# Performance work log

Hardware: AMD Instinct MI355X
Metric: run time of the kernel (lower is better)

The kernel has to match this reference:

```python
import jax, jax.numpy as jnp
import numpy as np
import math

N_HEAD = 16
HEAD_DIM = 64
LN_EPS = 1e-5
TEMP = 1.0

def _layernorm(x, scale, bias):
    # normalize over last dim (head_dim)
    mu = jnp.mean(x, axis=-1, keepdims=True)
    var = jnp.mean(jnp.square(x - mu), axis=-1, keepdims=True)
    return (x - mu) / jnp.sqrt(var + LN_EPS) * scale + bias

def setup_inputs() -> dict:
    key = jax.random.key(0)
    ks = jax.random.split(key, 3)
    B, S, C = 4, 2048, 1024
    x = jax.random.normal(ks[0], (B, S, C), dtype=jnp.float32)
    w_qkv = jax.random.normal(ks[1], (C, 3 * C), dtype=jnp.float32) * (C ** -0.5)
    w_proj = jax.random.normal(ks[2], (C, C), dtype=jnp.float32) * (C ** -0.5)
    return {
        "x": x,
        "w_qkv": w_qkv,
        "w_proj": w_proj,
        "q_scale": jnp.ones((HEAD_DIM,), jnp.float32),
        "q_bias": jnp.zeros((HEAD_DIM,), jnp.float32),
        "k_scale": jnp.ones((HEAD_DIM,), jnp.float32),
        "k_bias": jnp.zeros((HEAD_DIM,), jnp.float32),
    }

def reference(x, w_qkv, w_proj, q_scale, q_bias, k_scale, k_bias):
    B, S, C = x.shape
    H, D = N_HEAD, HEAD_DIM
    # qkv projection -> [B,S,3,H,D] -> [3,B,H,S,D]
    qkv = (x @ w_qkv).reshape(B, S, 3, H, D).transpose(2, 0, 3, 1, 4)
    q = _layernorm(qkv[0], q_scale, q_bias)
    k = _layernorm(qkv[1], k_scale, k_bias)
    v = qkv[2]
    # temperature-scaled logits, stable softmax
    inv = 1.0 / (math.sqrt(D) * max(TEMP, 1e-6))
    logits = jnp.einsum('bhqd,bhkd->bhqk', q, k) * inv
    att = jax.nn.softmax(logits, axis=-1)
    # entropy stats (track_stats=True path)
    s_raw = -jnp.sum(att * jnp.log(att + 1e-9), axis=-1)  # [B,H,S]
    batch_entropies = jnp.mean(s_raw / math.log(S), axis=(1, 2))  # [B]
    out = jnp.einsum('bhqk,bhkd->bhqd', att, v).transpose(0, 2, 1, 3).reshape(B, S, C)
    return out @ w_proj, batch_entropies
```

## Files before the change

kernel.cpp:

```cpp
#include <hip/hip_runtime.h>
#include <hip/hip_bf16.h>
#include <math.h>

#define CB 4
#define CS 2048
#define CC 1024
#define CH 16
#define CD 64
#define CBS (CB*CS)

typedef unsigned short u16;
typedef __bf16 bf16x8 __attribute__((ext_vector_type(8)));
typedef float f32x4 __attribute__((ext_vector_type(4)));
typedef float f32x16 __attribute__((ext_vector_type(16)));
typedef unsigned short u16x4 __attribute__((ext_vector_type(4)));
typedef unsigned short u16x8 __attribute__((ext_vector_type(8)));

__device__ __forceinline__ u16 f2bf(float f){
  union { float f; unsigned u; } v; v.f = f;
  unsigned r = v.u + 0x7FFFu + ((v.u >> 16) & 1u);
  return (u16)(r >> 16);
}
__device__ __forceinline__ unsigned pack2bf(float a, float b){
  __hip_bfloat162 h = __float22bfloat162_rn(make_float2(a, b));
  union { __hip_bfloat162 h; unsigned u; } c; c.h = h; return c.u;
}
__device__ __forceinline__ f32x4 mfma16(bf16x8 a, bf16x8 b, f32x4 c){
  return __builtin_amdgcn_mfma_f32_16x16x32_bf16(a, b, c, 0, 0, 0);
}
__device__ __forceinline__ f32x16 mfma32(bf16x8 a, bf16x8 b, f32x16 c){
  return __builtin_amdgcn_mfma_f32_32x32x16_bf16(a, b, c, 0, 0, 0);
}
__device__ __forceinline__ void gload16(const u16* g, u16* lds_base_uniform){
  __builtin_amdgcn_global_load_lds(
      (const __attribute__((address_space(1))) unsigned int*)g,
      (__attribute__((address_space(3))) unsigned int*)lds_base_uniform, 16, 0, 0);
}

__global__ __launch_bounds__(256) void convert_x_kernel(
    const float* __restrict__ x, u16* __restrict__ xb, float* __restrict__ zero4){
  if (blockIdx.x == 0 && threadIdx.x < 4) zero4[threadIdx.x] = 0.0f;
  size_t i = ((size_t)blockIdx.x*256 + threadIdx.x)*8;
  float4 a = *(const float4*)(x+i);
  float4 b = *(const float4*)(x+i+4);
  u16x8 o = { f2bf(a.x),f2bf(a.y),f2bf(a.z),f2bf(a.w),
              f2bf(b.x),f2bf(b.y),f2bf(b.z),f2bf(b.w) };
  *(u16x8*)(xb+i) = o;
}

template<int K, int N>
__global__ __launch_bounds__(256) void transpose_convert_kernel(
    const float* __restrict__ w, u16* __restrict__ wt){
  __shared__ u16 tile[64][65];
  const int nb = N/64;
  int tk0 = (blockIdx.x / nb) * 64;
  int tn0 = (blockIdx.x % nb) * 64;
  int t = threadIdx.x;
  for (int i = 0; i < 4; i++) {
    int r = i*16 + (t>>4);
    int c = (t&15)*4;
    float4 v = *(const float4*)(w + (size_t)(tk0+r)*N + tn0 + c);
    tile[c+0][r]=f2bf(v.x); tile[c+1][r]=f2bf(v.y);
    tile[c+2][r]=f2bf(v.z); tile[c+3][r]=f2bf(v.w);
  }
  __syncthreads();
  for (int i = 0; i < 4; i++) {
    int r = i*16 + (t>>4);
    int c = (t&15)*4;
    u16x4 o = { tile[r][c+0], tile[r][c+1], tile[r][c+2], tile[r][c+3] };
    *(u16x4*)(wt + (size_t)(tn0+r)*K + tk0 + c) = o;
  }
}

__global__ __launch_bounds__(256) void transpose_v_kernel(
    const u16* __restrict__ vb, u16* __restrict__ vtb){
  __shared__ u16 tile[64][72];
  int bh = blockIdx.x >> 5;
  int st = blockIdx.x & 31;
  int t = threadIdx.x;
  const u16* src = vb + (size_t)bh*CS*CD + (size_t)st*64*CD;
  int r = t>>2, c = (t&3)*16;
  *(u16x8*)&tile[r][c]   = *(const u16x8*)(src + (size_t)r*CD + c);
  *(u16x8*)&tile[r][c+8] = *(const u16x8*)(src + (size_t)r*CD + c + 8);
  __syncthreads();
  int d = t>>2, s = (t&3)*16;
  u16x8 o0, o1;
  for (int j=0;j<8;j++){ o0[j] = tile[s+j][d]; o1[j] = tile[s+8+j][d]; }
  u16* dst = vtb + (size_t)bh*CD*CS + (size_t)d*CS + st*64 + s;
  *(u16x8*)dst = o0;
  *(u16x8*)(dst+8) = o1;
}

__global__ __launch_bounds__(256, 2) void gemm_qkv_ln_kernel(
    const u16* __restrict__ xb, const u16* __restrict__ wqkvT,
    const float* __restrict__ qsc, const float* __restrict__ qbi,
    const float* __restrict__ ksc, const float* __restrict__ kbi,
    u16* __restrict__ qb, u16* __restrict__ kb, u16* __restrict__ vb){
  __shared__ u16 al[128*64];
  __shared__ u16 bl[128*64];
  int t = threadIdx.x;
  int wv = t >> 6, lane = t & 63, lo = lane & 15, q4 = lane >> 4;
  int m0 = blockIdx.x * 128;
  int n0 = blockIdx.y * 128;
  int srow = lane >> 3, scol = (lane & 7) * 8;
  const u16* ag = xb    + (size_t)(m0 + srow)*CC + scol;
  const u16* bg = wqkvT + (size_t)(n0 + srow)*CC + scol;

  f32x4 acc[2][8];
  for (int i=0;i<2;i++) for (int j=0;j<8;j++) acc[i][j] = (f32x4){0.f,0.f,0.f,0.f};

  for (int kk = 0; kk < 16; kk++){
    int k0 = kk * 64;
    for (int i = 0; i < 4; i++){
      int inst = i*4 + wv;
      gload16(ag + (size_t)inst*8*CC + k0, al + inst*512);
      gload16(bg + (size_t)inst*8*CC + k0, bl + inst*512);
    }
    __syncthreads();
    for (int ksI = 0; ksI < 2; ksI++){
      int koff = ksI*32 + q4*8;
      bf16x8 a0 = *(const bf16x8*)&al[(wv*32      + lo)*64 + koff];
      bf16x8 a1 = *(const bf16x8*)&al[(wv*32 + 16 + lo)*64 + koff];
      for (int nt=0; nt<8; nt++){
        bf16x8 b = *(const bf16x8*)&bl[(nt*16 + lo)*64 + koff];
        acc[0][nt] = mfma16(a0, b, acc[0][nt]);
        acc[1][nt] = mfma16(a1, b, acc[1][nt]);
      }
    }
    __syncthreads();
  }

  int three = n0 >> 10;
  int h0 = (n0 & 1023) >> 6;
  const float* scp = (three == 0) ? qsc : ksc;
  const float* bip = (three == 0) ? qbi : kbi;
  float outscale = (three == 0) ? 0.125f : 1.0f;
  u16* dst = (three == 0) ? qb : (three == 1 ? kb : vb);

  for (int rt = 0; rt < 2; rt++){
    int tg = m0 + wv*32 + rt*16 + q4*4;
    for (int hf = 0; hf < 2; hf++){
      int h = h0 + hf;
      for (int r = 0; r < 4; r++){
        int token = tg + r;
        int bb = token >> 11, ss = token & (CS-1);
        size_t base = (((size_t)(bb*CH + h))*CS + ss)*CD;
        if (three < 2){
          float s1 = 0.f, s2 = 0.f;
          for (int j=0;j<4;j++){ float v = acc[rt][hf*4+j][r]; s1 += v; s2 += v*v; }
          for (int off=8; off>=1; off>>=1){
            s1 += __shfl_xor(s1, off, 16);
            s2 += __shfl_xor(s2, off, 16);
          }
          float mean = s1 * (1.f/64.f);
          float var  = s2 * (1.f/64.f) - mean*mean;
          float rstd = rsqrtf(var + 1e-5f);
          for (int j=0;j<4;j++){
            int d = j*16 + lo;
            float v = (acc[rt][hf*4+j][r] - mean) * rstd * scp[d] + bip[d];
            dst[base + d] = f2bf(v * outscale);
          }
        } else {
          for (int j=0;j<4;j++){
            int d = j*16 + lo;
            dst[base + d] = f2bf(acc[rt][hf*4+j][r]);
          }
        }
      }
    }
  }
}

__global__ __launch_bounds__(256, 3) void attention_kernel(
    const u16* __restrict__ qb, const u16* __restrict__ kb,
    const u16* __restrict__ vtb, u16* __restrict__ attnb, float* __restrict__ ent){
  __shared__ __align__(16) u16 kl[2][64*64];
  __shared__ __align__(16) u16 vl[2][64*64];
  __shared__ __align__(16) u16 pl[4][32][72];
  __shared__ __align__(16) float zl[4][32];
  int t = threadIdx.x;
  int wv = t >> 6, lane = t & 63;
  int col = lane & 31, hi = lane >> 5;
  int n = blockIdx.x;
  int xc = n & 7, j = n >> 3;
  int bh = xc + 8*(j >> 4);
  int qt = j & 15;
  int bI = bh >> 4;
  int q0w = qt*128 + wv*32;
  const u16* qbp = qb  + (size_t)bh * CS * CD;
  const u16* kbp = kb  + (size_t)bh * CS * CD;
  const u16* vbp = vtb + (size_t)bh * CD * CS;

  int srow  = lane >> 3;
  int sslot = (lane & 7) ^ srow;

  bf16x8 qf[4];
  for (int ks=0;ks<4;ks++)
    qf[ks] = *(const bf16x8*)(qbp + (size_t)(q0w + col)*CD + ks*16 + hi*8);

  f32x16 o[2];
  for (int nt=0;nt<2;nt++) for (int i=0;i<16;i++) o[nt][i] = 0.f;
  float zacc = 0.f, tacc = 0.f;

  for (int c=0;c<2;c++){
    int chunk = wv*2 + c;
    int row = chunk*8 + srow;
    gload16(kbp + (size_t)row*CD + sslot*8, &kl[0][chunk*512]);
    gload16(vbp + (size_t)row*CS + sslot*8, &vl[0][chunk*512]);
  }

  const int cshift = (col & 7);

  for (int it = 0; it < 32; it++){
    const int cur = it & 1, nxt = cur ^ 1;
    __syncthreads();
    if (it < 31){
      int skn = (it+1)*64;
      for (int c=0;c<2;c++){
        int chunk = wv*2 + c;
        int row = chunk*8 + srow;
        gload16(kbp + (size_t)(skn + row)*CD + sslot*8, &kl[nxt][chunk*512]);
        gload16(vbp + (size_t)row*CS + skn + sslot*8, &vl[nxt][chunk*512]);
      }
    }

    bf16x8 kfr[2][4], vfr[2][4];
    for (int mt=0;mt<2;mt++)
      for (int ks=0;ks<4;ks++)
        kfr[mt][ks] = *(const bf16x8*)&kl[cur][(mt*32+col)*64 + (((2*ks+hi)^cshift)<<3)];
    for (int nt=0;nt<2;nt++)
      for (int ks=0;ks<4;ks++)
        vfr[nt][ks] = *(const bf16x8*)&vl[cur][(nt*32+col)*64 + (((2*ks+hi)^cshift)<<3)];

    f32x16 sf[2];
    for (int mt=0;mt<2;mt++) for (int i=0;i<16;i++) sf[mt][i] = 0.f;
    for (int ks=0;ks<4;ks++){
      sf[0] = mfma32(kfr[0][ks], qf[ks], sf[0]);
      sf[1] = mfma32(kfr[1][ks], qf[ks], sf[1]);
    }

    for (int mt=0;mt<2;mt++){
      for (int g=0; g<4; g++){
        float l0 = sf[mt][g*4+0], l1 = sf[mt][g*4+1],
              l2 = sf[mt][g*4+2], l3 = sf[mt][g*4+3];
        float p0=__expf(l0), p1=__expf(l1), p2=__expf(l2), p3=__expf(l3);
        zacc += (p0+p1)+(p2+p3);
        tacc += (p0*l0+p1*l1)+(p2*l2+p3*l3);
        union { u16x4 v; unsigned u[2]; } pk;
        pk.u[0] = pack2bf(p0, p1);
        pk.u[1] = pack2bf(p2, p3);
        *(u16x4*)&pl[wv][col][mt*32 + g*8 + hi*4] = pk.v;
      }
    }

    for (int ks=0;ks<4;ks++){
      bf16x8 ap = *(const bf16x8*)&pl[wv][col][ks*16 + hi*8];
      o[0] = mfma32(ap, vfr[0][ks], o[0]);
      o[1] = mfma32(ap, vfr[1][ks], o[1]);
    }
  }

  float z2 = zacc + __shfl_xor(zacc, 32);
  float t2 = tacc + __shfl_xor(tacc, 32);
  float invz = 1.f / z2;
  if (hi == 0) zl[wv][col] = invz;

  float srowv = __logf(z2) - t2 * invz;
  float ev = (hi == 0) ? srowv : 0.f;
  for (int off=1; off<=32; off<<=1) ev += __shfl_xor(ev, off);
  if (lane == 0){
    float entscale = 1.0f / ((float)CH * (float)CS * logf((float)CS));
    atomicAdd(&ent[bI], ev * entscale);
  }

  u16* obase = attnb + ((size_t)bh*CS + q0w)*CD;
  for (int nt=0;nt<2;nt++){
    for (int g=0;g<4;g++){
      f32x4 iz = *(const f32x4*)&zl[wv][g*8 + hi*4];
      for (int r=0;r<4;r++){
        int qrow = 8*g + 4*hi + r;
        obase[(size_t)qrow*CD + nt*32 + col] = f2bf(o[nt][g*4+r] * iz[r]);
      }
    }
  }
}

__global__ __launch_bounds__(256, 2) void gemm_out_kernel(
    const u16* __restrict__ attnH, const u16* __restrict__ wprojT,
    float* __restrict__ out){
  __shared__ u16 al[128*64];
  __shared__ u16 bl[128*64];
  int t = threadIdx.x;
  int wv = t >> 6, lane = t & 63, lo = lane & 15, q4 = lane >> 4;
  int m0 = blockIdx.x * 128;
  int n0 = blockIdx.y * 128;
  int b  = m0 >> 11, s0 = m0 & (CS-1);
  int srow = lane >> 3, scol = (lane & 7) * 8;
  const u16* bg = wprojT + (size_t)(n0 + srow)*CC + scol;

  f32x4 acc[2][8];
  for (int i=0;i<2;i++) for (int j=0;j<8;j++) acc[i][j] = (f32x4){0.f,0.f,0.f,0.f};

  for (int kk = 0; kk < 16; kk++){
    const u16* abase = attnH + ((size_t)(b*CH + kk)*CS + s0 + srow)*CD + scol;
    for (int i = 0; i < 4; i++){
      int inst = i*4 + wv;
      gload16(abase + (size_t)inst*8*CD, al + inst*512);
      gload16(bg + (size_t)inst*8*CC + kk*64, bl + inst*512);
    }
    __syncthreads();
    for (int ksI = 0; ksI < 2; ksI++){
      int koff = ksI*32 + q4*8;
      bf16x8 a0 = *(const bf16x8*)&al[(wv*32      + lo)*64 + koff];
      bf16x8 a1 = *(const bf16x8*)&al[(wv*32 + 16 + lo)*64 + koff];
      for (int nt=0; nt<8; nt++){
        bf16x8 b2 = *(const bf16x8*)&bl[(nt*16 + lo)*64 + koff];
        acc[0][nt] = mfma16(a0, b2, acc[0][nt]);
        acc[1][nt] = mfma16(a1, b2, acc[1][nt]);
      }
    }
    __syncthreads();
  }

  for (int rt=0;rt<2;rt++){
    for (int r=0;r<4;r++){
      int row = m0 + wv*32 + rt*16 + q4*4 + r;
      for (int nt=0;nt<8;nt++)
        out[(size_t)row*CC + n0 + nt*16 + lo] = acc[rt][nt][r];
    }
  }
}

extern "C" void kernel_launch(void* const* d_in, const int* in_sizes, int n_in,
                              void* d_out, int out_size, void* d_ws, size_t ws_size,
                              hipStream_t stream) {
  const float* x      = (const float*)d_in[0];
  const float* w_qkv  = (const float*)d_in[1];
  const float* w_proj = (const float*)d_in[2];
  const float* q_scale= (const float*)d_in[3];
  const float* q_bias = (const float*)d_in[4];
  const float* k_scale= (const float*)d_in[5];
  const float* k_bias = (const float*)d_in[6];
  float* out = (float*)d_out;
  float* ent = out + (size_t)CBS * CC;

  u16* xb     = (u16*)d_ws;
  u16* wqkvT  = xb     + (size_t)CBS*CC;
  u16* wprojT = wqkvT  + (size_t)3*CC*CC;
  u16* qb     = wprojT + (size_t)CC*CC;
  u16* kb     = qb + (size_t)CB*CH*CS*CD;
  u16* vb     = kb + (size_t)CB*CH*CS*CD;
  u16* vbT    = xb;
  u16* attn   = vb;

  convert_x_kernel<<<dim3(CBS*CC/(256*8)), 256, 0, stream>>>(x, xb, ent);
  transpose_convert_kernel<CC, 3*CC><<<dim3((CC/64)*(3*CC/64)), 256, 0, stream>>>(w_qkv, wqkvT);
  transpose_convert_kernel<CC, CC><<<dim3((CC/64)*(CC/64)), 256, 0, stream>>>(w_proj, wprojT);
  gemm_qkv_ln_kernel<<<dim3(CBS/128, 3*CC/128), 256, 0, stream>>>(
      xb, wqkvT, q_scale, q_bias, k_scale, k_bias, qb, kb, vb);
  transpose_v_kernel<<<dim3(CB*CH*(CS/64)), 256, 0, stream>>>(vb, vbT);
  attention_kernel<<<dim3(CB*CH*(CS/128)), 256, 0, stream>>>(qb, kb, vbT, attn, ent);
  gemm_out_kernel<<<dim3(CBS/128, CC/128), 256, 0, stream>>>(attn, wprojT, out);
}
```

Measured before the change: 355.4 us.

## Keep P in registers via permlane32 swap, use exp2 with folded log2e

Removes the per-wave LDS staging buffer for attention probabilities. The bf16 P fragments are now rearranged between lane halves with permlane32_swap so they feed the PV MFMA directly from registers. The log2(e) factor is folded into the q scaling so the kernel can call hardware exp2 and log2, with the entropy rescaled by ln2. Freeing LDS lets launch bounds rise from 3 to 4 blocks per SM, at some risk of register pressure.

```diff
diff --git a/kernel.cpp b/kernel.cpp
--- a/kernel.cpp
+++ b/kernel.cpp
@@ -15,6 +15,7 @@
 typedef float f32x16 __attribute__((ext_vector_type(16)));
 typedef unsigned short u16x4 __attribute__((ext_vector_type(4)));
 typedef unsigned short u16x8 __attribute__((ext_vector_type(8)));
+typedef unsigned u32x2 __attribute__((ext_vector_type(2)));
 
 __device__ __forceinline__ u16 f2bf(float f){
   union { float f; unsigned u; } v; v.f = f;
@@ -134,7 +135,7 @@
   int h0 = (n0 & 1023) >> 6;
   const float* scp = (three == 0) ? qsc : ksc;
   const float* bip = (three == 0) ? qbi : kbi;
-  float outscale = (three == 0) ? 0.125f : 1.0f;
+  float outscale = (three == 0) ? 0.125f * 1.44269504088896f : 1.0f;
   u16* dst = (three == 0) ? qb : (three == 1 ? kb : vb);
 
   for (int rt = 0; rt < 2; rt++){
@@ -171,12 +172,11 @@
   }
 }
 
-__global__ __launch_bounds__(256, 3) void attention_kernel(
+__global__ __launch_bounds__(256, 4) void attention_kernel(
     const u16* __restrict__ qb, const u16* __restrict__ kb,
     const u16* __restrict__ vtb, u16* __restrict__ attnb, float* __restrict__ ent){
   __shared__ __align__(16) u16 kl[2][64*64];
   __shared__ __align__(16) u16 vl[2][64*64];
-  __shared__ __align__(16) u16 pl[4][32][72];
   __shared__ __align__(16) float zl[4][32];
   int t = threadIdx.x;
   int wv = t >> 6, lane = t & 63;
@@ -240,23 +240,32 @@
     }
 
     for (int mt=0;mt<2;mt++){
-      for (int g=0; g<4; g++){
-        float l0 = sf[mt][g*4+0], l1 = sf[mt][g*4+1],
-              l2 = sf[mt][g*4+2], l3 = sf[mt][g*4+3];
-        float p0=__expf(l0), p1=__expf(l1), p2=__expf(l2), p3=__expf(l3);
-        zacc += (p0+p1)+(p2+p3);
-        tacc += (p0*l0+p1*l1)+(p2*l2+p3*l3);
-        union { u16x4 v; unsigned u[2]; } pk;
-        pk.u[0] = pack2bf(p0, p1);
-        pk.u[1] = pack2bf(p2, p3);
-        *(u16x4*)&pl[wv][col][mt*32 + g*8 + hi*4] = pk.v;
-      }
-    }
-
-    for (int ks=0;ks<4;ks++){
-      bf16x8 ap = *(const bf16x8*)&pl[wv][col][ks*16 + hi*8];
-      o[0] = mfma32(ap, vfr[0][ks], o[0]);
-      o[1] = mfma32(ap, vfr[1][ks], o[1]);
+      for (int ksl=0; ksl<2; ksl++){
+        float p[2][4];
+        for (int gg=0; gg<2; gg++){
+          int g = 2*ksl + gg;
+          float l0 = sf[mt][g*4+0], l1 = sf[mt][g*4+1],
+                l2 = sf[mt][g*4+2], l3 = sf[mt][g*4+3];
+          float p0 = __builtin_amdgcn_exp2f(l0);
+          float p1 = __builtin_amdgcn_exp2f(l1);
+          float p2 = __builtin_amdgcn_exp2f(l2);
+          float p3 = __builtin_amdgcn_exp2f(l3);
+          zacc += (p0+p1)+(p2+p3);
+          tacc += (p0*l0+p1*l1)+(p2*l2+p3*l3);
+          p[gg][0]=p0; p[gg][1]=p1; p[gg][2]=p2; p[gg][3]=p3;
+        }
+        unsigned x0 = pack2bf(p[0][0], p[0][1]);
+        unsigned x1 = pack2bf(p[0][2], p[0][3]);
+        unsigned y0 = pack2bf(p[1][0], p[1][1]);
+        unsigned y1 = pack2bf(p[1][2], p[1][3]);
+        u32x2 s0 = __builtin_amdgcn_permlane32_swap(x0, y0, false, false);
+        u32x2 s1 = __builtin_amdgcn_permlane32_swap(x1, y1, false, false);
+        union { unsigned u[4]; bf16x8 v; } ap;
+        ap.u[0] = s0[0]; ap.u[1] = s1[0]; ap.u[2] = s0[1]; ap.u[3] = s1[1];
+        int ks = mt*2 + ksl;
+        o[0] = mfma32(ap.v, vfr[0][ks], o[0]);
+        o[1] = mfma32(ap.v, vfr[1][ks], o[1]);
+      }
     }
   }
 
@@ -265,7 +274,7 @@
   float invz = 1.f / z2;
   if (hi == 0) zl[wv][col] = invz;
 
-  float srowv = __logf(z2) - t2 * invz;
+  float srowv = 0.69314718055995f * (__builtin_amdgcn_logf(z2) - t2 * invz);
   float ev = (hi == 0) ? srowv : 0.f;
   for (int off=1; off<=32; off<<=1) ev += __shfl_xor(ev, off);
   if (lane == 0){
```

New measurement: 359.0 us. No clear change (+1.0%).
